# Kernel tuning notes

Measured on AMD Instinct MI355X. Metric: run time of the kernel, lower is better.

Reference implementation:

```python
import jax, jax.numpy as jnp
import numpy as np

B, N_BUG, D_BUG, K, L, P = 2048, 2000, 30, 20, 40, 2
OMEGA_TEMP = 1.0


def setup_inputs() -> dict:
    key = jax.random.key(0)
    ks = jax.random.split(key, 14)
    f = lambda k, s, sc=1.0: sc * jax.random.normal(k, s, dtype=jnp.float32)
    return {
        "x": f(ks[0], (B, N_BUG)),
        "microbe_locs": f(ks[1], (N_BUG, D_BUG)),
        "mu_bug": f(ks[2], (L, D_BUG)),
        "r_bug": jax.random.uniform(ks[3], (L,), dtype=jnp.float32) * 20.0 + 10.0,
        "alpha": f(ks[4], (L, K)),
        "beta": f(ks[5], (K,)),
        "W1": f(ks[6], (K, L, P, 16), 0.5),
        "b1": f(ks[7], (K, L, P, 16), 0.1),
        "W2": f(ks[8], (K, L, P, 16, 16), 0.25),
        "b2": f(ks[9], (K, L, P, 16), 0.1),
        "W3": f(ks[10], (K, L, P, 16, 8), 0.25),
        "b3": f(ks[11], (K, L, P, 8), 0.1),
        "W4": f(ks[12], (K, L, P, 8), 0.35),
        "b4": f(ks[13], (K, L, P), 0.1),
    }


def reference(x, microbe_locs, mu_bug, r_bug, alpha, beta,
              W1, b1, W2, b2, W3, b3, W4, b4):
    # Distance-based soft microbe->cluster assignment (mu/r kernel):
    # kappa[m,l] = ||microbe_locs[m] - mu_bug[l]||^2
    kappa = jnp.sum((microbe_locs[:, None, :] - mu_bug[None, :, :]) ** 2, axis=-1)  # [N_bug, L]
    w_act = jax.nn.sigmoid((r_bug[None, :] - kappa) / OMEGA_TEMP)                  # [N_bug, L]
    g = x @ w_act                                                                   # [B, L] per-cluster microbe sums

    alpha_act = jax.nn.sigmoid(alpha)  # [L, K] soft edge selection

    # NAM: K*L*P independent tiny MLPs 1->16->16->8->1, batched over (k,l,p).
    h1 = jax.nn.elu(g[:, None, :, None, None] * W1[None] + b1[None])          # [B,K,L,P,16]
    h2 = jax.nn.elu(jnp.einsum('bklpi,klpij->bklpj', h1, W2) + b2[None])      # [B,K,L,P,16]
    h3 = jax.nn.elu(jnp.einsum('bklpi,klpij->bklpj', h2, W3) + b3[None])      # [B,K,L,P,8]
    f_out = jnp.einsum('bklpi,klpi->bklp', h3, W4) + b4[None]                 # [B,K,L,P]

    # out[b,k] = beta[k] + sum_l alpha_act[l,k] * sum_p f_out[b,k,l,p]
    out = beta[None, :] + jnp.einsum('bklp,lk->bk', f_out, alpha_act)         # [B,K]
    return out
```

## Files before the change

### kernel.cpp

```cpp
#include <hip/hip_runtime.h>
#include <hip/hip_bf16.h>

#define B_SZ 2048
#define NB   2000
#define DB   30
#define KK   20
#define LL   40
#define PP   2

typedef _Float16 f16x4 __attribute__((ext_vector_type(4)));
typedef float    f32x4 __attribute__((ext_vector_type(4)));

#define BLOB_F 336

__device__ __forceinline__ float sigmoidf_fast(float z) {
    return 1.0f / (1.0f + __expf(-z));
}
__device__ __forceinline__ float eluf(float x) {
    return x > 0.0f ? x : (__expf(x) - 1.0f);
}

__global__ __launch_bounds__(64) void beta_kern(
    const float* __restrict__ alpha, const float* __restrict__ beta,
    const float* __restrict__ b4, float* __restrict__ beta_eff)
{
    int k = threadIdx.x;
    if (k < KK) {
        float s = beta[k];
        for (int l = 0; l < LL; ++l) {
            float a = sigmoidf_fast(alpha[l * KK + k]);
            s += a * (b4[(k * LL + l) * PP + 0] + b4[(k * LL + l) * PP + 1]);
        }
        beta_eff[k] = s;
    }
}

__global__ __launch_bounds__(256) void prep_kern(
    const float* __restrict__ locs, const float* __restrict__ mu,
    const float* __restrict__ r, const float* __restrict__ beta_eff,
    float* __restrict__ w_act, float* __restrict__ out)
{
    __shared__ float smu[LL * DB];
    __shared__ float sr[LL];
    int tid = threadIdx.x;
    for (int t = tid; t < LL * DB; t += 256) smu[t] = mu[t];
    if (tid < LL) sr[tid] = r[tid];
    __syncthreads();

    int gid = blockIdx.x * 256 + tid;
    if (gid < NB * LL) {
        int m = gid / LL;
        int l = gid - m * LL;
        float kappa = 0.0f;
        #pragma unroll
        for (int d = 0; d < DB; ++d) {
            float diff = locs[m * DB + d] - smu[l * DB + d];
            kappa += diff * diff;
        }
        w_act[gid] = sigmoidf_fast(sr[l] - kappa);
    }
    if (gid < B_SZ * KK) out[gid] = beta_eff[gid % KK];
}

__global__ __launch_bounds__(64) void repack_kern(
    const float* __restrict__ alpha,
    const float* __restrict__ W1, const float* __restrict__ b1,
    const float* __restrict__ W2, const float* __restrict__ b2,
    const float* __restrict__ W3, const float* __restrict__ b3,
    const float* __restrict__ W4, float* __restrict__ blob)
{
    int bid = blockIdx.x;
    int k = bid / (PP * LL);
    int rem = bid - k * (PP * LL);
    int p = rem / LL;
    int l = rem - p * LL;
    int iw = (k * LL + l) * PP + p;
    int t = threadIdx.x;
    int n = t & 15, q = t >> 4;
    float* o = blob + (size_t)bid * BLOB_F;

    float aact = sigmoidf_fast(alpha[l * KK + k]);

    if (t < 16) {
        o[t]      = W1[iw * 16 + t];
        o[16 + t] = b1[iw * 16 + t];
        o[32 + t] = b2[iw * 16 + t];
        o[48 + t] = (t < 8) ? b3[iw * 8 + t] : 0.0f;
        o[64 + t] = (t < 8) ? W4[iw * 8 + t] * aact : 0.0f;
    }
    _Float16* w2a = (_Float16*)(o + 80);
    #pragma unroll
    for (int j = 0; j < 4; ++j)
        w2a[t * 4 + j] = (_Float16)W2[iw * 256 + (4 * q + j) * 16 + n];
    _Float16* w3a = (_Float16*)(o + 208);
    #pragma unroll
    for (int j = 0; j < 4; ++j)
        w3a[t * 4 + j] = (n < 8) ? (_Float16)W3[iw * 128 + (4 * q + j) * 8 + n]
                                 : (_Float16)0.0f;
}

__global__ __launch_bounds__(256) void g_kern(
    const float* __restrict__ x,
    const float* __restrict__ w_act,
    float* __restrict__ g_part)
{
    __shared__ float  xs[64 * 127];
    __shared__ float4 ws4[1250];

    int bb = blockIdx.x & 31;
    int mq = blockIdx.x >> 5;
    int tid = threadIdx.x;
    int i = tid & 63;
    int w = tid >> 6;

    float acc[10];
    #pragma unroll
    for (int u = 0; u < 10; ++u) acc[u] = 0.0f;

    for (int c = 0; c < 2; ++c) {
        int m0 = mq * 250 + c * 125;
        __syncthreads();
        for (int t = tid; t < 64 * 125; t += 256) {
            int ii = t / 125;
            int jj = t - ii * 125;
            xs[ii * 127 + jj] = x[(bb * 64 + ii) * NB + m0 + jj];
        }
        {
            const float4* wa4 = (const float4*)w_act;
            for (int t = tid; t < 1250; t += 256)
                ws4[t] = wa4[m0 * 10 + t];
        }
        __syncthreads();
        const float* wsf = (const float*)ws4;
        #pragma unroll 5
        for (int m = 0; m < 125; ++m) {
            float xv = xs[i * 127 + m];
            const float* wrow = &wsf[m * LL + w * 10];
            #pragma unroll
            for (int u = 0; u < 10; ++u)
                acc[u] += xv * wrow[u];
        }
    }
    #pragma unroll
    for (int u = 0; u < 10; ++u)
        g_part[((size_t)mq * LL + w * 10 + u) * B_SZ + bb * 64 + i] = acc[u];
}

__global__ __launch_bounds__(256) void g_reduce(
    const float* __restrict__ g_part, float* __restrict__ g_T)
{
    int t = blockIdx.x * 256 + threadIdx.x;
    float s = 0.0f;
    #pragma unroll
    for (int mq = 0; mq < 8; ++mq)
        s += g_part[(size_t)mq * LL * B_SZ + t];
    g_T[t] = s;
}

__global__ __launch_bounds__(256) void nam_kern(
    const float* __restrict__ g_T,
    const float* __restrict__ blob,
    float* __restrict__ out)
{
    __shared__ __align__(16) float sw[10 * BLOB_F];

    int bid = blockIdx.x;
    int bb = bid & 15;
    int lc = (bid >> 4) & 3;
    int p  = (bid >> 6) & 1;
    int k  = bid >> 7;
    int tid = threadIdx.x;

    {
        const float4* bl4 = (const float4*)blob;
        float4* sw4 = (float4*)sw;
        size_t base = ((size_t)(k * PP + p) * LL + lc * 10) * (BLOB_F / 4);
        for (int t = tid; t < 10 * (BLOB_F / 4); t += 256)
            sw4[t] = bl4[base + t];
    }
    __syncthreads();

    int wv = tid >> 6;
    int lane = tid & 63;
    int n = lane & 15;
    int q = lane >> 4;
    int b0 = bb * 128 + wv * 32 + n;

    float acc0 = 0.0f, acc1 = 0.0f;
    const f32x4 zero = {0.0f, 0.0f, 0.0f, 0.0f};

    #pragma unroll 1
    for (int u = 0; u < 10; ++u) {
        const float* W = sw + u * BLOB_F;
        f32x4 w1q = *(const f32x4*)(W + q * 4);
        f32x4 b1q = *(const f32x4*)(W + 16 + q * 4);
        f32x4 b2q = *(const f32x4*)(W + 32 + q * 4);
        f32x4 b3q = *(const f32x4*)(W + 48 + q * 4);
        f32x4 w4q = *(const f32x4*)(W + 64 + q * 4);
        f16x4 w2a = *(const f16x4*)((const _Float16*)(W + 80) + lane * 4);
        f16x4 w3a = *(const f16x4*)((const _Float16*)(W + 208) + lane * 4);

        int l = lc * 10 + u;
        float g0 = g_T[l * B_SZ + b0];
        float g1 = g_T[l * B_SZ + b0 + 16];

        f16x4 hb0, hb1;
        #pragma unroll
        for (int j = 0; j < 4; ++j) {
            hb0[j] = (_Float16)eluf(fmaf(g0, w1q[j], b1q[j]));
            hb1[j] = (_Float16)eluf(fmaf(g1, w1q[j], b1q[j]));
        }

        f32x4 d20 = __builtin_amdgcn_mfma_f32_16x16x16f16(w2a, hb0, zero, 0, 0, 0);
        f32x4 d21 = __builtin_amdgcn_mfma_f32_16x16x16f16(w2a, hb1, zero, 0, 0, 0);

        f16x4 hc0, hc1;
        #pragma unroll
        for (int j = 0; j < 4; ++j) {
            hc0[j] = (_Float16)eluf(d20[j] + b2q[j]);
            hc1[j] = (_Float16)eluf(d21[j] + b2q[j]);
        }

        f32x4 d30 = __builtin_amdgcn_mfma_f32_16x16x16f16(w3a, hc0, zero, 0, 0, 0);
        f32x4 d31 = __builtin_amdgcn_mfma_f32_16x16x16f16(w3a, hc1, zero, 0, 0, 0);

        #pragma unroll
        for (int r = 0; r < 4; ++r) {
            acc0 = fmaf(eluf(d30[r] + b3q[r]), w4q[r], acc0);
            acc1 = fmaf(eluf(d31[r] + b3q[r]), w4q[r], acc1);
        }
    }

    acc0 += __shfl_xor(acc0, 16, 64);
    acc0 += __shfl_xor(acc0, 32, 64);
    acc1 += __shfl_xor(acc1, 16, 64);
    acc1 += __shfl_xor(acc1, 32, 64);
    if (lane < 16) {
        atomicAdd(&out[(size_t)b0 * KK + k], acc0);
        atomicAdd(&out[(size_t)(b0 + 16) * KK + k], acc1);
    }
}

extern "C" void kernel_launch(void* const* d_in, const int* in_sizes, int n_in,
                              void* d_out, int out_size, void* d_ws, size_t ws_size,
                              hipStream_t stream) {
    const float* x     = (const float*)d_in[0];
    const float* locs  = (const float*)d_in[1];
    const float* mu    = (const float*)d_in[2];
    const float* r     = (const float*)d_in[3];
    const float* alpha = (const float*)d_in[4];
    const float* beta  = (const float*)d_in[5];
    const float* W1    = (const float*)d_in[6];
    const float* b1    = (const float*)d_in[7];
    const float* W2    = (const float*)d_in[8];
    const float* b2    = (const float*)d_in[9];
    const float* W3    = (const float*)d_in[10];
    const float* b3    = (const float*)d_in[11];
    const float* W4    = (const float*)d_in[12];
    const float* b4    = (const float*)d_in[13];
    float* out = (float*)d_out;

    float* ws0      = (float*)d_ws;
    float* w_act    = ws0;
    float* g_T      = w_act + NB * LL;
    float* g_part   = g_T + LL * B_SZ;
    float* blob     = g_part + (size_t)8 * LL * B_SZ;
    float* beta_eff = blob + (size_t)KK * PP * LL * BLOB_F;

    beta_kern<<<1, 64, 0, stream>>>(alpha, beta, b4, beta_eff);
    prep_kern<<<320, 256, 0, stream>>>(locs, mu, r, beta_eff, w_act, out);
    repack_kern<<<KK * PP * LL, 64, 0, stream>>>(alpha, W1, b1, W2, b2, W3, b3, W4, blob);
    g_kern<<<256, 256, 0, stream>>>(x, w_act, g_part);
    g_reduce<<<320, 256, 0, stream>>>(g_part, g_T);
    nam_kern<<<2560, 256, 0, stream>>>(g_T, blob, out);
}
```

Baseline: 158.0 us.

## Fuse all stages into one cooperative persistent kernel with grid syncs

Replaces the six separate launches (beta, prep, repack, g matmul, reduce, NAM) with a single cooperative kernel of 1024 blocks that separates phases with grid.sync(). It also re-tiles the x@w_act stage into 16 m-chunks with smaller 32-row tiles so all blocks participate, and folds the b2/b3 biases into the MFMA accumulator inputs. The intent is to remove launch gaps and improve occupancy of the small phases, at the cost of grid-wide barriers, a larger partial-sum buffer to reduce, and a redundant zeroing of g_part.

```diff
diff --git a/kernel.cpp b/kernel.cpp
--- a/kernel.cpp
+++ b/kernel.cpp
@@ -1,5 +1,8 @@
 #include <hip/hip_runtime.h>
 #include <hip/hip_bf16.h>
+#include <hip/hip_cooperative_groups.h>
+
+namespace cg = cooperative_groups;
 
 #define B_SZ 2048
 #define NB   2000
@@ -8,11 +11,15 @@
 #define LL   40
 #define PP   2
 
+#define BLOB_F 336
+
+#define GRID_SZ 1024
+#define NMQ 16
+#define NUNITS_C 2560
+
 typedef _Float16 f16x4 __attribute__((ext_vector_type(4)));
 typedef float    f32x4 __attribute__((ext_vector_type(4)));
 
-#define BLOB_F 336
-
 __device__ __forceinline__ float sigmoidf_fast(float z) {
     return 1.0f / (1.0f + __expf(-z));
 }
@@ -20,12 +27,81 @@
     return x > 0.0f ? x : (__expf(x) - 1.0f);
 }
 
-__global__ __launch_bounds__(64) void beta_kern(
+union SmemU {
+    struct { float smu[LL * DB]; float sr[LL]; } a;
+    struct { float xs[32 * 27]; float ws[25 * LL]; } b;
+    float sw[10 * BLOB_F];
+};
+
+__global__ __launch_bounds__(256, 4) void fused_kern(
+    const float* __restrict__ x, const float* __restrict__ locs,
+    const float* __restrict__ mu, const float* __restrict__ r,
     const float* __restrict__ alpha, const float* __restrict__ beta,
-    const float* __restrict__ b4, float* __restrict__ beta_eff)
+    const float* __restrict__ W1, const float* __restrict__ b1,
+    const float* __restrict__ W2, const float* __restrict__ b2,
+    const float* __restrict__ W3, const float* __restrict__ b3,
+    const float* __restrict__ W4, const float* __restrict__ b4,
+    float* __restrict__ w_act, float* __restrict__ g_T,
+    float* __restrict__ g_part, float* __restrict__ blob,
+    float* __restrict__ beta_eff, float* __restrict__ out)
 {
-    int k = threadIdx.x;
-    if (k < KK) {
+    cg::grid_group grid = cg::this_grid();
+    __shared__ SmemU sm;
+    const int tid  = threadIdx.x;
+    const int bidx = blockIdx.x;
+    const int vt   = bidx * 256 + tid;
+
+    {
+        const float4 z = {0.0f, 0.0f, 0.0f, 0.0f};
+        float4* gp4 = (float4*)g_part;
+        for (int j = vt; j < (NMQ * LL * B_SZ) / 4; j += GRID_SZ * 256)
+            gp4[j] = z;
+    }
+    if (bidx < 320) {
+        for (int t = tid; t < LL * DB; t += 256) sm.a.smu[t] = mu[t];
+        if (tid < LL) sm.a.sr[tid] = r[tid];
+        __syncthreads();
+        if (vt < NB * LL) {
+            int m = vt / LL;
+            int l = vt - m * LL;
+            float kappa = 0.0f;
+            #pragma unroll
+            for (int d = 0; d < DB; ++d) {
+                float diff = locs[m * DB + d] - sm.a.smu[l * DB + d];
+                kappa += diff * diff;
+            }
+            w_act[vt] = sigmoidf_fast(sm.a.sr[l] - kappa);
+        }
+    } else if (vt >= 81920 && vt < 184320) {
+        int vt2 = vt - 81920;
+        int bidb = vt2 >> 6;
+        int t = vt2 & 63;
+        int k = bidb / (PP * LL);
+        int rem = bidb - k * (PP * LL);
+        int p = rem / LL;
+        int l = rem - p * LL;
+        int iw = (k * LL + l) * PP + p;
+        int n = t & 15, q = t >> 4;
+        float* o = blob + (size_t)bidb * BLOB_F;
+        float aact = sigmoidf_fast(alpha[l * KK + k]);
+        if (t < 16) {
+            o[t]      = W1[iw * 16 + t];
+            o[16 + t] = b1[iw * 16 + t];
+            o[32 + t] = b2[iw * 16 + t];
+            o[48 + t] = (t < 8) ? b3[iw * 8 + t] : 0.0f;
+            o[64 + t] = (t < 8) ? W4[iw * 8 + t] * aact : 0.0f;
+        }
+        _Float16* w2a = (_Float16*)(o + 80);
+        #pragma unroll
+        for (int j = 0; j < 4; ++j)
+            w2a[t * 4 + j] = (_Float16)W2[iw * 256 + (4 * q + j) * 16 + n];
+        _Float16* w3a = (_Float16*)(o + 208);
+        #pragma unroll
+        for (int j = 0; j < 4; ++j)
+            w3a[t * 4 + j] = (n < 8) ? (_Float16)W3[iw * 128 + (4 * q + j) * 8 + n]
+                                     : (_Float16)0.0f;
+    } else if (vt >= 184320 && vt < 184320 + KK) {
+        int k = vt - 184320;
         float s = beta[k];
         for (int l = 0; l < LL; ++l) {
             float a = sigmoidf_fast(alpha[l * KK + k]);
@@ -33,211 +109,123 @@
         }
         beta_eff[k] = s;
     }
-}
-
-__global__ __launch_bounds__(256) void prep_kern(
-    const float* __restrict__ locs, const float* __restrict__ mu,
-    const float* __restrict__ r, const float* __restrict__ beta_eff,
-    float* __restrict__ w_act, float* __restrict__ out)
-{
-    __shared__ float smu[LL * DB];
-    __shared__ float sr[LL];
-    int tid = threadIdx.x;
-    for (int t = tid; t < LL * DB; t += 256) smu[t] = mu[t];
-    if (tid < LL) sr[tid] = r[tid];
-    __syncthreads();
-
-    int gid = blockIdx.x * 256 + tid;
-    if (gid < NB * LL) {
-        int m = gid / LL;
-        int l = gid - m * LL;
-        float kappa = 0.0f;
-        #pragma unroll
-        for (int d = 0; d < DB; ++d) {
-            float diff = locs[m * DB + d] - smu[l * DB + d];
-            kappa += diff * diff;
-        }
-        w_act[gid] = sigmoidf_fast(sr[l] - kappa);
-    }
-    if (gid < B_SZ * KK) out[gid] = beta_eff[gid % KK];
-}
-
-__global__ __launch_bounds__(64) void repack_kern(
-    const float* __restrict__ alpha,
-    const float* __restrict__ W1, const float* __restrict__ b1,
-    const float* __restrict__ W2, const float* __restrict__ b2,
-    const float* __restrict__ W3, const float* __restrict__ b3,
-    const float* __restrict__ W4, float* __restrict__ blob)
-{
-    int bid = blockIdx.x;
-    int k = bid / (PP * LL);
-    int rem = bid - k * (PP * LL);
-    int p = rem / LL;
-    int l = rem - p * LL;
-    int iw = (k * LL + l) * PP + p;
-    int t = threadIdx.x;
-    int n = t & 15, q = t >> 4;
-    float* o = blob + (size_t)bid * BLOB_F;
-
-    float aact = sigmoidf_fast(alpha[l * KK + k]);
-
-    if (t < 16) {
-        o[t]      = W1[iw * 16 + t];
-        o[16 + t] = b1[iw * 16 + t];
-        o[32 + t] = b2[iw * 16 + t];
-        o[48 + t] = (t < 8) ? b3[iw * 8 + t] : 0.0f;
-        o[64 + t] = (t < 8) ? W4[iw * 8 + t] * aact : 0.0f;
-    }
-    _Float16* w2a = (_Float16*)(o + 80);
-    #pragma unroll
-    for (int j = 0; j < 4; ++j)
-        w2a[t * 4 + j] = (_Float16)W2[iw * 256 + (4 * q + j) * 16 + n];
-    _Float16* w3a = (_Float16*)(o + 208);
-    #pragma unroll
-    for (int j = 0; j < 4; ++j)
-        w3a[t * 4 + j] = (n < 8) ? (_Float16)W3[iw * 128 + (4 * q + j) * 8 + n]
-                                 : (_Float16)0.0f;
-}
-
-__global__ __launch_bounds__(256) void g_kern(
-    const float* __restrict__ x,
-    const float* __restrict__ w_act,
-    float* __restrict__ g_part)
-{
-    __shared__ float  xs[64 * 127];
-    __shared__ float4 ws4[1250];
-
-    int bb = blockIdx.x & 31;
-    int mq = blockIdx.x >> 5;
-    int tid = threadIdx.x;
-    int i = tid & 63;
-    int w = tid >> 6;
-
-    float acc[10];
-    #pragma unroll
-    for (int u = 0; u < 10; ++u) acc[u] = 0.0f;
-
-    for (int c = 0; c < 2; ++c) {
-        int m0 = mq * 250 + c * 125;
-        __syncthreads();
-        for (int t = tid; t < 64 * 125; t += 256) {
-            int ii = t / 125;
-            int jj = t - ii * 125;
-            xs[ii * 127 + jj] = x[(bb * 64 + ii) * NB + m0 + jj];
-        }
-        {
-            const float4* wa4 = (const float4*)w_act;
-            for (int t = tid; t < 1250; t += 256)
-                ws4[t] = wa4[m0 * 10 + t];
-        }
-        __syncthreads();
-        const float* wsf = (const float*)ws4;
-        #pragma unroll 5
-        for (int m = 0; m < 125; ++m) {
-            float xv = xs[i * 127 + m];
-            const float* wrow = &wsf[m * LL + w * 10];
-            #pragma unroll
-            for (int u = 0; u < 10; ++u)
-                acc[u] += xv * wrow[u];
-        }
-    }
-    #pragma unroll
-    for (int u = 0; u < 10; ++u)
-        g_part[((size_t)mq * LL + w * 10 + u) * B_SZ + bb * 64 + i] = acc[u];
-}
-
-__global__ __launch_bounds__(256) void g_reduce(
-    const float* __restrict__ g_part, float* __restrict__ g_T)
-{
-    int t = blockIdx.x * 256 + threadIdx.x;
-    float s = 0.0f;
-    #pragma unroll
-    for (int mq = 0; mq < 8; ++mq)
-        s += g_part[(size_t)mq * LL * B_SZ + t];
-    g_T[t] = s;
-}
-
-__global__ __launch_bounds__(256) void nam_kern(
-    const float* __restrict__ g_T,
-    const float* __restrict__ blob,
-    float* __restrict__ out)
-{
-    __shared__ __align__(16) float sw[10 * BLOB_F];
-
-    int bid = blockIdx.x;
-    int bb = bid & 15;
-    int lc = (bid >> 4) & 3;
-    int p  = (bid >> 6) & 1;
-    int k  = bid >> 7;
-    int tid = threadIdx.x;
+    grid.sync();
 
     {
-        const float4* bl4 = (const float4*)blob;
-        float4* sw4 = (float4*)sw;
-        size_t base = ((size_t)(k * PP + p) * LL + lc * 10) * (BLOB_F / 4);
-        for (int t = tid; t < 10 * (BLOB_F / 4); t += 256)
-            sw4[t] = bl4[base + t];
-    }
-    __syncthreads();
-
-    int wv = tid >> 6;
-    int lane = tid & 63;
-    int n = lane & 15;
-    int q = lane >> 4;
-    int b0 = bb * 128 + wv * 32 + n;
-
-    float acc0 = 0.0f, acc1 = 0.0f;
-    const f32x4 zero = {0.0f, 0.0f, 0.0f, 0.0f};
-
-    #pragma unroll 1
-    for (int u = 0; u < 10; ++u) {
-        const float* W = sw + u * BLOB_F;
-        f32x4 w1q = *(const f32x4*)(W + q * 4);
-        f32x4 b1q = *(const f32x4*)(W + 16 + q * 4);
-        f32x4 b2q = *(const f32x4*)(W + 32 + q * 4);
-        f32x4 b3q = *(const f32x4*)(W + 48 + q * 4);
-        f32x4 w4q = *(const f32x4*)(W + 64 + q * 4);
-        f16x4 w2a = *(const f16x4*)((const _Float16*)(W + 80) + lane * 4);
-        f16x4 w3a = *(const f16x4*)((const _Float16*)(W + 208) + lane * 4);
-
-        int l = lc * 10 + u;
-        float g0 = g_T[l * B_SZ + b0];
-        float g1 = g_T[l * B_SZ + b0 + 16];
-
-        f16x4 hb0, hb1;
-        #pragma unroll
-        for (int j = 0; j < 4; ++j) {
-            hb0[j] = (_Float16)eluf(fmaf(g0, w1q[j], b1q[j]));
-            hb1[j] = (_Float16)eluf(fmaf(g1, w1q[j], b1q[j]));
-        }
-
-        f32x4 d20 = __builtin_amdgcn_mfma_f32_16x16x16f16(w2a, hb0, zero, 0, 0, 0);
-        f32x4 d21 = __builtin_amdgcn_mfma_f32_16x16x16f16(w2a, hb1, zero, 0, 0, 0);
-
-        f16x4 hc0, hc1;
-        #pragma unroll
-        for (int j = 0; j < 4; ++j) {
-            hc0[j] = (_Float16)eluf(d20[j] + b2q[j]);
-            hc1[j] = (_Float16)eluf(d21[j] + b2q[j]);
-        }
-
-        f32x4 d30 = __builtin_amdgcn_mfma_f32_16x16x16f16(w3a, hc0, zero, 0, 0, 0);
-        f32x4 d31 = __builtin_amdgcn_mfma_f32_16x16x16f16(w3a, hc1, zero, 0, 0, 0);
-
-        #pragma unroll
-        for (int r = 0; r < 4; ++r) {
-            acc0 = fmaf(eluf(d30[r] + b3q[r]), w4q[r], acc0);
-            acc1 = fmaf(eluf(d31[r] + b3q[r]), w4q[r], acc1);
-        }
-    }
-
-    acc0 += __shfl_xor(acc0, 16, 64);
-    acc0 += __shfl_xor(acc0, 32, 64);
-    acc1 += __shfl_xor(acc1, 16, 64);
-    acc1 += __shfl_xor(acc1, 32, 64);
-    if (lane < 16) {
-        atomicAdd(&out[(size_t)b0 * KK + k], acc0);
-        atomicAdd(&out[(size_t)(b0 + 16) * KK + k], acc1);
+        int bb = bidx >> 4;
+        int mq = bidx & 15;
+        int i  = tid & 31;
+        int gq = tid >> 5;
+        float acc[5] = {0, 0, 0, 0, 0};
+        for (int c = 0; c < 5; ++c) {
+            int m0 = mq * 125 + c * 25;
+            __syncthreads();
+            for (int t = tid; t < 32 * 25; t += 256) {
+                int ii = t / 25, jj = t - ii * 25;
+                sm.b.xs[ii * 27 + jj] = x[(bb * 32 + ii) * NB + m0 + jj];
+            }
+            {
+                const float4* wa4 = (const float4*)(w_act + m0 * LL);
+                float4* dst = (float4*)sm.b.ws;
+                for (int t = tid; t < 250; t += 256) dst[t] = wa4[t];
+            }
+            __syncthreads();
+            #pragma unroll 5
+            for (int m = 0; m < 25; ++m) {
+                float xv = sm.b.xs[i * 27 + m];
+                const float* wrow = &sm.b.ws[m * LL + gq * 5];
+                #pragma unroll
+                for (int u = 0; u < 5; ++u)
+                    acc[u] = fmaf(xv, wrow[u], acc[u]);
+            }
+        }
+        #pragma unroll
+        for (int u = 0; u < 5; ++u)
+            g_part[(mq * LL + gq * 5 + u) * B_SZ + bb * 32 + i] = acc[u];
+    }
+    grid.sync();
+
+    for (int j = vt; j < LL * B_SZ; j += GRID_SZ * 256) {
+        float s = 0.0f;
+        #pragma unroll
+        for (int mq = 0; mq < NMQ; ++mq)
+            s += g_part[mq * LL * B_SZ + j];
+        g_T[j] = s;
+    }
+    for (int j = vt; j < B_SZ * KK; j += GRID_SZ * 256)
+        out[j] = beta_eff[j % KK];
+    grid.sync();
+
+    {
+        const int wv = tid >> 6, lane = tid & 63;
+        const int n = lane & 15, q = lane >> 4;
+        for (int unit = bidx; unit < NUNITS_C; unit += GRID_SZ) {
+            int bb = unit & 15;
+            int rr = unit >> 4;
+            int lc = rr & 3, p = (rr >> 2) & 1, k = rr >> 3;
+            __syncthreads();
+            {
+                const float4* bl4 = (const float4*)blob;
+                float4* sw4 = (float4*)sm.sw;
+                int base = ((k * PP + p) * LL + lc * 10) * (BLOB_F / 4);
+                for (int t = tid; t < 10 * (BLOB_F / 4); t += 256)
+                    sw4[t] = bl4[base + t];
+            }
+            __syncthreads();
+            int b0 = bb * 128 + wv * 32 + n;
+            float acc0 = 0.0f, acc1 = 0.0f;
+
+            #pragma unroll 1
+            for (int u = 0; u < 10; ++u) {
+                const float* W = sm.sw + u * BLOB_F;
+                f32x4 w1q = *(const f32x4*)(W + q * 4);
+                f32x4 b1q = *(const f32x4*)(W + 16 + q * 4);
+                f32x4 b2q = *(const f32x4*)(W + 32 + q * 4);
+                f32x4 b3q = *(const f32x4*)(W + 48 + q * 4);
+                f32x4 w4q = *(const f32x4*)(W + 64 + q * 4);
+                f16x4 w2a = *(const f16x4*)((const _Float16*)(W + 80) + lane * 4);
+                f16x4 w3a = *(const f16x4*)((const _Float16*)(W + 208) + lane * 4);
+
+                int l = lc * 10 + u;
+                float g0 = g_T[l * B_SZ + b0];
+                float g1 = g_T[l * B_SZ + b0 + 16];
+
+                f16x4 hb0, hb1;
+                #pragma unroll
+                for (int j = 0; j < 4; ++j) {
+                    hb0[j] = (_Float16)eluf(fmaf(g0, w1q[j], b1q[j]));
+                    hb1[j] = (_Float16)eluf(fmaf(g1, w1q[j], b1q[j]));
+                }
+
+                f32x4 d20 = __builtin_amdgcn_mfma_f32_16x16x16f16(w2a, hb0, b2q, 0, 0, 0);
+                f32x4 d21 = __builtin_amdgcn_mfma_f32_16x16x16f16(w2a, hb1, b2q, 0, 0, 0);
+
+                f16x4 hc0, hc1;
+                #pragma unroll
+                for (int j = 0; j < 4; ++j) {
+                    hc0[j] = (_Float16)eluf(d20[j]);
+                    hc1[j] = (_Float16)eluf(d21[j]);
+                }
+
+                f32x4 d30 = __builtin_amdgcn_mfma_f32_16x16x16f16(w3a, hc0, b3q, 0, 0, 0);
+                f32x4 d31 = __builtin_amdgcn_mfma_f32_16x16x16f16(w3a, hc1, b3q, 0, 0, 0);
+
+                #pragma unroll
+                for (int rj = 0; rj < 4; ++rj) {
+                    acc0 = fmaf(eluf(d30[rj]), w4q[rj], acc0);
+                    acc1 = fmaf(eluf(d31[rj]), w4q[rj], acc1);
+                }
+            }
+
+            acc0 += __shfl_xor(acc0, 16, 64);
+            acc0 += __shfl_xor(acc0, 32, 64);
+            acc1 += __shfl_xor(acc1, 16, 64);
+            acc1 += __shfl_xor(acc1, 32, 64);
+            if (lane < 16) {
+                atomicAdd(&out[b0 * KK + k], acc0);
+                atomicAdd(&out[(b0 + 16) * KK + k], acc1);
+            }
+        }
     }
 }
 
@@ -264,13 +252,16 @@
     float* w_act    = ws0;
     float* g_T      = w_act + NB * LL;
     float* g_part   = g_T + LL * B_SZ;
-    float* blob     = g_part + (size_t)8 * LL * B_SZ;
+    float* blob     = g_part + (size_t)NMQ * LL * B_SZ;
     float* beta_eff = blob + (size_t)KK * PP * LL * BLOB_F;
 
-    beta_kern<<<1, 64, 0, stream>>>(alpha, beta, b4, beta_eff);
-    prep_kern<<<320, 256, 0, stream>>>(locs, mu, r, beta_eff, w_act, out);
-    repack_kern<<<KK * PP * LL, 64, 0, stream>>>(alpha, W1, b1, W2, b2, W3, b3, W4, blob);
-    g_kern<<<256, 256, 0, stream>>>(x, w_act, g_part);
-    g_reduce<<<320, 256, 0, stream>>>(g_part, g_T);
-    nam_kern<<<2560, 256, 0, stream>>>(g_T, blob, out);
-}
+    void* args[] = {
+        (void*)&x, (void*)&locs, (void*)&mu, (void*)&r, (void*)&alpha,
+        (void*)&beta, (void*)&W1, (void*)&b1, (void*)&W2, (void*)&b2,
+        (void*)&W3, (void*)&b3, (void*)&W4, (void*)&b4,
+        (void*)&w_act, (void*)&g_T, (void*)&g_part, (void*)&blob,
+        (void*)&beta_eff, (void*)&out
+    };
+    hipLaunchCooperativeKernel((const void*)fused_kern, dim3(GRID_SZ), dim3(256),
+                               args, 0, stream);
+}
```

New measurement: 501.9 us. 218% more time.
